# Kernel tuning notes

Measured on AMD Instinct MI355X. Metric: run time of the kernel, lower is better.

Reference implementation:

```python
import jax, jax.numpy as jnp
import numpy as np

N = 6144      # num_sample / nodes per graph
E = 196608    # edges per graph (avg degree 32)
F = 256       # input feature dim (same for all 4 graphs)
H = 256       # hidden_channels (== F so all SAGEConv layers are HxH)
D = 512       # fusion dim (hardcoded in module)
G = 4         # number of graphs
ATT = 128     # attention bottleneck (hardcoded)
WS = 0.05     # weight init scale


def setup_inputs() -> dict:
    key = jax.random.key(0)
    k = jax.random.split(key, 16)
    return {
        "xs": jax.random.normal(k[0], (G, N, F), jnp.float32),
        "edge_index": jax.random.randint(k[1], (G, 2, E), 0, N),
        "x_content": jax.random.normal(k[2], (N, F), jnp.float32),
        # SAGEConv params: per graph, 3 layers, lin_l (with bias) on aggregated
        # neighbors, lin_r (no bias) on root. F == H so all layers stack.
        "sage_Wl": jax.random.normal(k[3], (G, 3, H, H), jnp.float32) * WS,
        "sage_bl": jnp.zeros((G, 3, H), jnp.float32),
        "sage_Wr": jax.random.normal(k[4], (G, 3, H, H), jnp.float32) * WS,
        # lin1..lin4 : F -> 512
        "lin_W": jax.random.normal(k[5], (G, D, F), jnp.float32) * WS,
        "lin_b": jnp.zeros((G, D), jnp.float32),
        # ResidualFusion attention MLP 512 -> 128 -> 1, softmax over graph axis
        "att_W1": jax.random.normal(k[6], (ATT, D), jnp.float32) * WS,
        "att_b1": jnp.zeros((ATT,), jnp.float32),
        "att_W2": jax.random.normal(k[7], (1, ATT), jnp.float32) * WS,
        "att_b2": jnp.zeros((1,), jnp.float32),
        "res_W": jax.random.normal(k[8], (D, D), jnp.float32) * WS,
        "res_b": jnp.zeros((D,), jnp.float32),
        "fusion_weight": jnp.array([0.7, 0.3], jnp.float32),
        # SelfExpression coefficients, init 1e-8 * ones as in the module
        "C_content": jnp.full((N, N), 1e-8, jnp.float32),
        "C_structure": jnp.full((N, N), 1e-8, jnp.float32),
    }


def _gnn(x, ei, Wl, bl, Wr):
    # One GraphSAGE stack: 3 SAGEConv(mean) layers, relu after each,
    # dropout is identity in eval mode.
    src, dst = ei[0], ei[1]
    deg = jax.ops.segment_sum(jnp.ones((E,), x.dtype), dst, num_segments=N)
    deg = jnp.maximum(deg, 1.0)[:, None]
    for i in range(3):
        m = jax.ops.segment_sum(x[src], dst, num_segments=N) / deg  # mean aggr
        x = jax.nn.relu(m @ Wl[i].T + bl[i] + x @ Wr[i].T)
    return x


def reference(xs, edge_index, x_content, sage_Wl, sage_bl, sage_Wr,
              lin_W, lin_b, att_W1, att_b1, att_W2, att_b2,
              res_W, res_b, fusion_weight, C_content, C_structure):
    # Four GraphSAGE stacks, vmapped over the graph axis.
    xg = jax.vmap(_gnn)(xs, edge_index, sage_Wl, sage_bl, sage_Wr)  # [G,N,F]
    # lin1..lin4 -> [G,N,D]
    feats = jnp.einsum('gnf,gdf->gnd', xg, lin_W) + lin_b[:, None, :]
    # ResidualFusion: attention over stacked features, softmax over graph axis
    h = jax.nn.relu(jnp.einsum('gnd,kd->gnk', feats, att_W1) + att_b1)
    logits = jnp.einsum('gnk,ok->gno', h, att_W2) + att_b2  # [G,N,1]
    w = jax.nn.softmax(logits, axis=0)
    weighted = jnp.sum(w * feats, axis=0)            # [N,D]
    residual = feats[0] @ res_W.T + res_b            # [N,D]
    structure_features = jax.nn.relu(weighted + residual)
    # Coefficient fusion with softmax-normalized scalar weights
    fw = jax.nn.softmax(fusion_weight)
    fusion_expression = fw[0] * C_content + fw[1] * C_structure  # [N,N]
    return (fusion_expression, x_content, structure_features, C_content, C_structure)
```

## Files before the change

kernel.cpp:

```cpp
#include <hip/hip_runtime.h>
#include <hip/hip_bf16.h>

constexpr int N_ = 6144;
constexpr int E_ = 196608;
constexpr int F_ = 256;
constexpr int D_ = 512;
constexpr int G_ = 4;
constexpr int A_ = 128;

typedef short bf16x8 __attribute__((ext_vector_type(8)));
typedef float f32x4 __attribute__((ext_vector_type(4)));
typedef float f4 __attribute__((ext_vector_type(4)));
typedef int i4 __attribute__((ext_vector_type(4)));
typedef __hip_bfloat16 hb;

__device__ inline float b2f(unsigned short u) {
    union { unsigned u32; float f; } x; x.u32 = ((unsigned)u) << 16; return x.f;
}
__device__ inline unsigned short f2bu(float f) {
    hb b = __float2bfloat16(f);
    return *reinterpret_cast<unsigned short*>(&b);
}

#define GLD_LDS16(gp, lp) \
    __builtin_amdgcn_global_load_lds((const __attribute__((address_space(1))) void*)(gp), \
                                     (__attribute__((address_space(3))) void*)(lp), 16, 0, 0)

struct SP {
    const f4* Cc; const f4* Cs; const float* fw;
    f4* o0; f4* o3; f4* o4;
    long ib; long ie; int nsb;
};

__device__ void stream_slice(const SP sp, int sb)
{
    float fa = sp.fw[0], fb = sp.fw[1];
    float mx = fmaxf(fa, fb);
    float ea = expf(fa - mx), eb = expf(fb - mx);
    float w0 = ea / (ea + eb), w1 = eb / (ea + eb);
    const long S = (long)sp.nsb * blockDim.x;
    long i = sp.ib + (long)sb * blockDim.x + threadIdx.x;
    for (; i + 3 * S < sp.ie; i += 4 * S) {
        f4 a0 = __builtin_nontemporal_load(sp.Cc + i);
        f4 b0 = __builtin_nontemporal_load(sp.Cs + i);
        f4 a1 = __builtin_nontemporal_load(sp.Cc + i + S);
        f4 b1 = __builtin_nontemporal_load(sp.Cs + i + S);
        f4 a2 = __builtin_nontemporal_load(sp.Cc + i + 2 * S);
        f4 b2 = __builtin_nontemporal_load(sp.Cs + i + 2 * S);
        f4 a3 = __builtin_nontemporal_load(sp.Cc + i + 3 * S);
        f4 b3 = __builtin_nontemporal_load(sp.Cs + i + 3 * S);
        __builtin_nontemporal_store(a0, sp.o3 + i);
        __builtin_nontemporal_store(b0, sp.o4 + i);
        __builtin_nontemporal_store(w0 * a0 + w1 * b0, sp.o0 + i);
        __builtin_nontemporal_store(a1, sp.o3 + i + S);
        __builtin_nontemporal_store(b1, sp.o4 + i + S);
        __builtin_nontemporal_store(w0 * a1 + w1 * b1, sp.o0 + i + S);
        __builtin_nontemporal_store(a2, sp.o3 + i + 2 * S);
        __builtin_nontemporal_store(b2, sp.o4 + i + 2 * S);
        __builtin_nontemporal_store(w0 * a2 + w1 * b2, sp.o0 + i + 2 * S);
        __builtin_nontemporal_store(a3, sp.o3 + i + 3 * S);
        __builtin_nontemporal_store(b3, sp.o4 + i + 3 * S);
        __builtin_nontemporal_store(w0 * a3 + w1 * b3, sp.o0 + i + 3 * S);
    }
    for (; i < sp.ie; i += S) {
        f4 a = __builtin_nontemporal_load(sp.Cc + i);
        f4 b = __builtin_nontemporal_load(sp.Cs + i);
        __builtin_nontemporal_store(a, sp.o3 + i);
        __builtin_nontemporal_store(b, sp.o4 + i);
        __builtin_nontemporal_store(w0 * a + w1 * b, sp.o0 + i);
    }
}

__global__ void k_tail(SP sp) { stream_slice(sp, blockIdx.x); }

__global__ void k_prep(const float* __restrict__ xc, f4* __restrict__ o1,
                       const float* __restrict__ xs, ushort4* __restrict__ xsb,
                       const float* __restrict__ Wl, ushort4* __restrict__ Wlb,
                       const float* __restrict__ Wr, ushort4* __restrict__ Wrb,
                       const float* __restrict__ lin, ushort4* __restrict__ linb,
                       const float* __restrict__ aw, ushort4* __restrict__ awb,
                       const float* __restrict__ rw, ushort4* __restrict__ rwb,
                       i4* __restrict__ cursz, int PB, SP sp)
{
    if ((int)blockIdx.x >= PB) { stream_slice(sp, blockIdx.x - PB); return; }
    const long nz = (long)G_ * N_ / 4;
    const long n0 = (long)N_ * F_ / 4;
    const long n1 = (long)G_ * N_ * F_ / 4;
    const long n2 = (long)G_ * 3 * F_ * F_ / 4;
    const long n4 = (long)G_ * D_ * F_ / 4;
    const long n5 = (long)A_ * D_ / 4;
    const long n6 = (long)D_ * D_ / 4;
    const long T = nz + n0 + n1 + 2 * n2 + n4 + n5 + n6;
    long stride = (long)PB * blockDim.x;
    for (long u = (long)blockIdx.x * blockDim.x + threadIdx.x; u < T; u += stride) {
        long v = u;
        if (v < nz) { cursz[v] = i4{0, 0, 0, 0}; continue; }
        v -= nz;
        if (v < n0) {
            f4 x = __builtin_nontemporal_load((const f4*)xc + v);
            __builtin_nontemporal_store(x, o1 + v);
            continue;
        }
        v -= n0;
        const float* s; ushort4* d;
        if (v < n1) { s = xs; d = xsb; }
        else {
            v -= n1;
            if (v < n2) { s = Wl; d = Wlb; }
            else {
                v -= n2;
                if (v < n2) { s = Wr; d = Wrb; }
                else {
                    v -= n2;
                    if (v < n4) { s = lin; d = linb; }
                    else {
                        v -= n4;
                        if (v < n5) { s = aw; d = awb; }
                        else { v -= n5; s = rw; d = rwb; }
                    }
                }
            }
        }
        f4 x = *((const f4*)s + v);
        ushort4 o;
        o.x = f2bu(x[0]); o.y = f2bu(x[1]); o.z = f2bu(x[2]); o.w = f2bu(x[3]);
        d[v] = o;
    }
}

__global__ void k_count(const int* __restrict__ ei, int* __restrict__ cnt, SP sp)
{
    if ((int)blockIdx.x >= G_ * E_ / 256) { stream_slice(sp, blockIdx.x - G_ * E_ / 256); return; }
    long i = (long)blockIdx.x * blockDim.x + threadIdx.x;
    int g = (int)(i / E_);
    int e = (int)(i % E_);
    int dst = ei[(long)g * 2 * E_ + E_ + e];
    atomicAdd(&cnt[g * N_ + dst], 1);
}

__global__ void k_scan(int* __restrict__ cnt_cursor, int* __restrict__ row_ptr,
                       float* __restrict__ deg, SP sp)
{
    if ((int)blockIdx.x >= G_) { stream_slice(sp, blockIdx.x - G_); return; }
    int g = blockIdx.x;
    __shared__ int sdata[1024];
    __shared__ int s_off;
    if (threadIdx.x == 0) s_off = 0;
    __syncthreads();
    for (int base = 0; base < N_; base += 1024) {
        int idx = g * N_ + base + threadIdx.x;
        int v = cnt_cursor[idx];
        sdata[threadIdx.x] = v;
        __syncthreads();
        for (int d = 1; d < 1024; d <<= 1) {
            int t = (threadIdx.x >= d) ? sdata[threadIdx.x - d] : 0;
            __syncthreads();
            sdata[threadIdx.x] += t;
            __syncthreads();
        }
        int incl = sdata[threadIdx.x];
        int excl = incl - v;
        int rp = s_off + excl;
        row_ptr[g * (N_ + 1) + base + threadIdx.x] = rp;
        cnt_cursor[idx] = rp;
        deg[idx] = (float)(v > 1 ? v : 1);
        __syncthreads();
        if (threadIdx.x == 1023) s_off += incl;
        __syncthreads();
    }
    if (threadIdx.x == 0) row_ptr[g * (N_ + 1) + N_] = s_off;
}

__global__ void k_fill(const int* __restrict__ ei, int* __restrict__ cursor,
                       int* __restrict__ csr_src, SP sp)
{
    if ((int)blockIdx.x >= G_ * E_ / 256) { stream_slice(sp, blockIdx.x - G_ * E_ / 256); return; }
    long i = (long)blockIdx.x * blockDim.x + threadIdx.x;
    int g = (int)(i / E_);
    int e = (int)(i % E_);
    int src = ei[(long)g * 2 * E_ + e];
    int dst = ei[(long)g * 2 * E_ + E_ + e];
    int pos = atomicAdd(&cursor[g * N_ + dst], 1);
    csr_src[(long)g * E_ + pos] = src;
}

__global__ __launch_bounds__(256) void k_aggregate(
    const hb* __restrict__ x, const int* __restrict__ csr_src,
    const int* __restrict__ row_ptr, const float* __restrict__ deg,
    hb* __restrict__ m, SP sp)
{
    int b = blockIdx.x;
    if (b >= G_ * N_ / 4) { stream_slice(sp, b - G_ * N_ / 4); return; }
    int g = (b & 7) >> 1;
    int idx = ((b >> 3) << 1) | (b & 1);
    int node = idx * 4 + (threadIdx.x >> 6);
    int lane = threadIdx.x & 63;
    int qq = lane >> 4;
    int l16 = (lane & 15) * 16;
    const hb* xg = x + (long)g * N_ * F_;
    const int* rp = row_ptr + g * (N_ + 1);
    const int* cs = csr_src + (long)g * E_;
    int s = __builtin_amdgcn_readfirstlane(rp[node]);
    int e = __builtin_amdgcn_readfirstlane(rp[node + 1]);
    float a[16] = {};
    #pragma unroll 2
    for (int j = s; j < e; j += 4) {
        if (j + qq < e) {
            int src = cs[j + qq];
            const bf16x8* p = (const bf16x8*)(xg + (long)src * F_ + l16);
            bf16x8 v0 = p[0], v1 = p[1];
            #pragma unroll
            for (int q = 0; q < 8; ++q) a[q]     += b2f((unsigned short)v0[q]);
            #pragma unroll
            for (int q = 0; q < 8; ++q) a[q + 8] += b2f((unsigned short)v1[q]);
        }
    }
    #pragma unroll
    for (int q = 0; q < 16; ++q) {
        a[q] += __shfl_xor(a[q], 16);
        a[q] += __shfl_xor(a[q], 32);
    }
    if (qq == 0) {
        float inv = 1.0f / deg[g * N_ + node];
        bf16x8 lo, hi;
        #pragma unroll
        for (int q = 0; q < 8; ++q) { lo[q] = (short)f2bu(a[q] * inv); hi[q] = (short)f2bu(a[q + 8] * inv); }
        *(bf16x8*)(m + ((long)g * N_ + node) * F_ + l16) = lo;
        *(bf16x8*)(m + ((long)g * N_ + node) * F_ + l16 + 8) = hi;
    }
}

template <bool DUAL, bool RELU, bool LOGITS, bool FUSEOUT, bool PIN>
__global__ __launch_bounds__(256) void k_mfma_nt(
    const hb* __restrict__ A1, const hb* __restrict__ B1,
    const hb* __restrict__ A2, const hb* __restrict__ B2,
    const float* __restrict__ bias, hb* __restrict__ C,
    int ncols, int nrows, int ng, int Nc, int K,
    long a_batch, long b_batch, long bias_batch, long c_batch,
    const float* __restrict__ W2, const float* __restrict__ b2,
    float* __restrict__ logits,
    const float* __restrict__ lgAll, const hb* __restrict__ fAll,
    float* __restrict__ o2,
    SP sp)
{
    const int nComp = ncols * nrows * ng;
    int b = blockIdx.x;
    if (b >= nComp) { stream_slice(sp, b - nComp); return; }
    int g, col, row;
    if (PIN) {
        g = (b & 7) >> 1;
        int idx = ((b >> 3) << 1) | (b & 1);
        col = idx % ncols; row = idx / ncols;
    } else {
        col = b % ncols;
        int r2 = b / ncols;
        row = r2 % nrows; g = r2 / nrows;
    }
    const int row0 = row * 128;
    const int col0 = col * 128;

    const hb* A1p = A1 + (long)g * a_batch;
    const hb* B1p = B1 + (long)g * b_batch;
    const hb* A2p = nullptr;
    const hb* B2p = nullptr;
    if (DUAL) { A2p = A2 + (long)g * a_batch; B2p = B2 + (long)g * b_batch; }
    const float* biasp = bias + (long)g * bias_batch;
    hb* Cp = C + (long)g * c_batch;

    __shared__ hb As[128 * 64];
    __shared__ hb Bs[128 * 64];
    __shared__ float sLog[2][128];
    __shared__ float sW[128][4];

    const int tid = threadIdx.x;
    const int lane = tid & 63;
    const int wid = tid >> 6;
    const int wr = wid >> 1;
    const int wc = wid & 1;

    if (FUSEOUT) {
        if (tid < 128) {
            int rr = row0 + tid;
            float l0 = lgAll[rr], l1 = lgAll[N_ + rr], l2 = lgAll[2 * N_ + rr], l3 = lgAll[3 * N_ + rr];
            float mx = fmaxf(fmaxf(l0, l1), fmaxf(l2, l3));
            float e0 = expf(l0 - mx), e1 = expf(l1 - mx), e2 = expf(l2 - mx), e3 = expf(l3 - mx);
            float inv = 1.f / (e0 + e1 + e2 + e3);
            sW[tid][0] = e0 * inv; sW[tid][1] = e1 * inv;
            sW[tid][2] = e2 * inv; sW[tid][3] = e3 * inv;
        }
    }

    const int srow = tid >> 3;
    const int sk8  = (tid & 7) * 8;

    f32x4 acc[4][4] = {};

    const int fr  = lane & 15;
    const int fkq = (lane >> 4) * 8;

    const int npass = DUAL ? 2 : 1;
    for (int pass = 0; pass < npass; ++pass) {
        const hb* A = (DUAL && pass) ? A2p : A1p;
        const hb* B = (DUAL && pass) ? B2p : B1p;
        for (int k0 = 0; k0 < K; k0 += 64) {
            __syncthreads();
            #pragma unroll
            for (int c = 0; c < 4; ++c) {
                int r = c * 32 + srow;
                GLD_LDS16(A + (long)(row0 + r) * K + k0 + sk8, As + r * 64 + sk8);
                GLD_LDS16(B + (long)(col0 + r) * K + k0 + sk8, Bs + r * 64 + sk8);
            }
            __syncthreads();

            bf16x8 af[4][2], bfr[4][2];
            #pragma unroll
            for (int m = 0; m < 4; ++m)
                #pragma unroll
                for (int kk = 0; kk < 2; ++kk)
                    af[m][kk] = *(const bf16x8*)(As + (wr * 64 + m * 16 + fr) * 64 + kk * 32 + fkq);
            #pragma unroll
            for (int n = 0; n < 4; ++n)
                #pragma unroll
                for (int kk = 0; kk < 2; ++kk)
                    bfr[n][kk] = *(const bf16x8*)(Bs + (wc * 64 + n * 16 + fr) * 64 + kk * 32 + fkq);

            #pragma unroll
            for (int m = 0; m < 4; ++m)
                #pragma unroll
                for (int n = 0; n < 4; ++n)
                    #pragma unroll
                    for (int kk = 0; kk < 2; ++kk)
                        acc[m][n] = __builtin_amdgcn_mfma_f32_16x16x32_bf16(
                            af[m][kk], bfr[n][kk], acc[m][n], 0, 0, 0);
        }
    }

    const int r4 = (lane >> 4) * 4;
    const int cc = lane & 15;

    if (LOGITS) {
        float w2v[4], bv[4];
        #pragma unroll
        for (int n = 0; n < 4; ++n) {
            int c2 = wc * 64 + n * 16 + cc;
            w2v[n] = W2[c2];
            bv[n]  = biasp[c2];
        }
        #pragma unroll
        for (int m = 0; m < 4; ++m) {
            #pragma unroll
            for (int j = 0; j < 4; ++j) {
                float p = 0.f;
                #pragma unroll
                for (int n = 0; n < 4; ++n) {
                    float h = fmaxf(acc[m][n][j] + bv[n], 0.f);
                    p += h * w2v[n];
                }
                p += __shfl_xor(p, 1); p += __shfl_xor(p, 2);
                p += __shfl_xor(p, 4); p += __shfl_xor(p, 8);
                if (cc == 0) sLog[wc][wr * 64 + m * 16 + r4 + j] = p;
            }
        }
        __syncthreads();
        if (tid < 128)
            logits[(long)g * N_ + row0 + tid] = sLog[0][tid] + sLog[1][tid] + b2[0];
    } else if (FUSEOUT) {
        const unsigned short* fu = (const unsigned short*)fAll;
        #pragma unroll
        for (int m = 0; m < 4; ++m) {
            #pragma unroll
            for (int n = 0; n < 4; ++n) {
                int c2 = col0 + wc * 64 + n * 16 + cc;
                float bv = biasp[c2];
                #pragma unroll
                for (int j = 0; j < 4; ++j) {
                    int rl = wr * 64 + m * 16 + r4 + j;
                    int rr = row0 + rl;
                    float s = acc[m][n][j] + bv;
                    #pragma unroll
                    for (int gg = 0; gg < 4; ++gg)
                        s += sW[rl][gg] * b2f(fu[((long)gg * N_ + rr) * D_ + c2]);
                    __builtin_nontemporal_store(fmaxf(s, 0.f), o2 + (long)rr * D_ + c2);
                }
            }
        }
    } else {
        #pragma unroll
        for (int m = 0; m < 4; ++m) {
            #pragma unroll
            for (int n = 0; n < 4; ++n) {
                int c2 = col0 + wc * 64 + n * 16 + cc;
                float bv = biasp[c2];
                #pragma unroll
                for (int j = 0; j < 4; ++j) {
                    int rr = row0 + wr * 64 + m * 16 + r4 + j;
                    float v = acc[m][n][j] + bv;
                    if (RELU) v = fmaxf(v, 0.f);
                    Cp[(long)rr * Nc + c2] = __float2bfloat16(v);
                }
            }
        }
    }
}

extern "C" void kernel_launch(void* const* d_in, const int* in_sizes, int n_in,
                              void* d_out, int out_size, void* d_ws, size_t ws_size,
                              hipStream_t stream)
{
    const float* xs        = (const float*)d_in[0];
    const int*   ei        = (const int*)  d_in[1];
    const float* x_content = (const float*)d_in[2];
    const float* sage_Wl   = (const float*)d_in[3];
    const float* sage_bl   = (const float*)d_in[4];
    const float* sage_Wr   = (const float*)d_in[5];
    const float* lin_W     = (const float*)d_in[6];
    const float* lin_b     = (const float*)d_in[7];
    const float* att_W1    = (const float*)d_in[8];
    const float* att_b1    = (const float*)d_in[9];
    const float* att_W2    = (const float*)d_in[10];
    const float* att_b2    = (const float*)d_in[11];
    const float* res_W     = (const float*)d_in[12];
    const float* res_b     = (const float*)d_in[13];
    const float* fusion_w  = (const float*)d_in[14];
    const float* Cc        = (const float*)d_in[15];
    const float* Cs        = (const float*)d_in[16];

    float* out0 = (float*)d_out;
    float* out1 = out0 + (size_t)N_ * N_;
    float* out2 = out1 + (size_t)N_ * F_;
    float* out3 = out2 + (size_t)N_ * D_;
    float* out4 = out3 + (size_t)N_ * N_;

    char* w = (char*)d_ws;
    auto alloc = [&](size_t bytes) {
        char* p = w;
        w += (bytes + 255) & ~(size_t)255;
        return p;
    };
    hb* xsb   = (hb*)alloc((size_t)G_ * N_ * F_ * 2);
    hb* xA    = (hb*)alloc((size_t)G_ * N_ * F_ * 2);
    hb* xB    = (hb*)alloc((size_t)G_ * N_ * F_ * 2);
    hb* mb    = (hb*)alloc((size_t)G_ * N_ * F_ * 2);
    hb* feats = (hb*)alloc((size_t)G_ * N_ * D_ * 2);
    hb* Wlb   = (hb*)alloc((size_t)G_ * 3 * F_ * F_ * 2);
    hb* Wrb   = (hb*)alloc((size_t)G_ * 3 * F_ * F_ * 2);
    hb* linWb = (hb*)alloc((size_t)G_ * D_ * F_ * 2);
    hb* attWb = (hb*)alloc((size_t)A_ * D_ * 2);
    hb* resWb = (hb*)alloc((size_t)D_ * D_ * 2);
    float* logit = (float*)alloc((size_t)G_ * N_ * 4);
    float* deg   = (float*)alloc((size_t)G_ * N_ * 4);
    int*   rowp  = (int*)  alloc((size_t)G_ * (N_ + 1) * 4);
    int*   curs  = (int*)  alloc((size_t)G_ * N_ * 4);
    int*   csrc  = (int*)  alloc((size_t)G_ * E_ * 4);

    const long U = (long)N_ * N_ / 4;
    const int cum[14] = {0, 100, 115, 123, 143, 183, 233, 273, 323, 363, 413, 468, 648, 898};
    long B[14];
    for (int i = 0; i < 14; ++i) B[i] = U * cum[i] / 1000;
    const int PREPB   = 512;
    const int SB_PREP = 512;
    const int SB_FLAT = 256;
    const int SB_GEMM = 256;
    const int SB_ATT  = 768;
    const int SB_RES  = 1024;
    const int TAILB   = 1024;
    auto mkSP = [&](int i, int nsb) {
        SP sp;
        sp.Cc = (const f4*)Cc; sp.Cs = (const f4*)Cs; sp.fw = fusion_w;
        sp.o0 = (f4*)out0; sp.o3 = (f4*)out3; sp.o4 = (f4*)out4;
        sp.ib = B[i]; sp.ie = (i == 13) ? U : B[i + 1]; sp.nsb = nsb;
        return sp;
    };
    SP tail = mkSP(13, TAILB);

    k_prep<<<PREPB + SB_PREP, 256, 0, stream>>>(
        x_content, (f4*)out1, xs, (ushort4*)xsb,
        sage_Wl, (ushort4*)Wlb, sage_Wr, (ushort4*)Wrb,
        lin_W, (ushort4*)linWb, att_W1, (ushort4*)attWb, res_W, (ushort4*)resWb,
        (i4*)curs, PREPB, mkSP(0, SB_PREP));

    k_count<<<G_ * E_ / 256 + SB_FLAT, 256, 0, stream>>>(ei, curs, mkSP(1, SB_FLAT));
    k_scan<<<G_ + SB_FLAT, 1024, 0, stream>>>(curs, rowp, deg, mkSP(2, SB_FLAT));
    k_fill<<<G_ * E_ / 256 + SB_FLAT, 256, 0, stream>>>(ei, curs, csrc, mkSP(3, SB_FLAT));

    const hb* xin = xsb;
    hb* xout = xA;
    for (int layer = 0; layer < 3; ++layer) {
        k_aggregate<<<G_ * N_ / 4 + SB_FLAT, 256, 0, stream>>>(
            xin, csrc, rowp, deg, mb, mkSP(4 + 2 * layer, SB_FLAT));
        k_mfma_nt<true, true, false, false, true>
            <<<(F_ / 128) * (N_ / 128) * G_ + SB_GEMM, 256, 0, stream>>>(
            mb, Wlb + (size_t)layer * F_ * F_,
            xin, Wrb + (size_t)layer * F_ * F_,
            sage_bl + (size_t)layer * F_, xout,
            F_ / 128, N_ / 128, G_, F_, F_,
            (long)N_ * F_, (long)3 * F_ * F_, (long)3 * F_, (long)N_ * F_,
            nullptr, nullptr, nullptr, nullptr, nullptr, nullptr,
            mkSP(5 + 2 * layer, SB_GEMM));
        xin = xout;
        xout = (layer == 0) ? xB : xA;
    }
    const hb* xg = xA;

    k_mfma_nt<false, false, false, false, true>
        <<<(D_ / 128) * (N_ / 128) * G_ + SB_GEMM, 256, 0, stream>>>(
        xg, linWb, nullptr, nullptr, lin_b, feats,
        D_ / 128, N_ / 128, G_, D_, F_,
        (long)N_ * F_, (long)D_ * F_, (long)D_, (long)N_ * D_,
        nullptr, nullptr, nullptr, nullptr, nullptr, nullptr,
        mkSP(10, SB_GEMM));

    k_mfma_nt<false, true, true, false, true>
        <<<(A_ / 128) * (N_ / 128) * G_ + SB_ATT, 256, 0, stream>>>(
        feats, attWb, nullptr, nullptr, att_b1, nullptr,
        A_ / 128, N_ / 128, G_, A_, D_,
        (long)N_ * D_, 0L, 0L, 0L,
        att_W2, att_b2, logit, nullptr, nullptr, nullptr,
        mkSP(11, SB_ATT));

    k_mfma_nt<false, false, false, true, false>
        <<<(D_ / 128) * (N_ / 128) * 1 + SB_RES, 256, 0, stream>>>(
        feats, resWb, nullptr, nullptr, res_b, nullptr,
        D_ / 128, N_ / 128, 1, D_, D_,
        0L, 0L, 0L, 0L,
        nullptr, nullptr, nullptr, logit, feats, out2,
        mkSP(12, SB_RES));

    k_tail<<<TAILB, 256, 0, stream>>>(tail);
}
```

Before: 433.9 us.

## Replace static copy-stream slices with atomic work-stealing chunks across all kernels

The large N×N coefficient copy/blend stream was split into hand-tuned fixed fractions per kernel launch. It is now claimed in 16K-float4 chunks through a global atomic cursor that every kernel's extra blocks, and compute blocks once their own work is done, drain dynamically. The aim is to balance the bandwidth-bound stream against compute phases without hand-tuned ratios and to shrink the final tail kernel. This costs an atomic and two block barriers per chunk, and compute blocks may linger in the stream and delay the next dependent launch.

```diff
diff --git a/kernel.cpp b/kernel.cpp
--- a/kernel.cpp
+++ b/kernel.cpp
@@ -8,6 +8,10 @@
 constexpr int G_ = 4;
 constexpr int A_ = 128;
 
+constexpr int CHUNK_F4 = 16384;
+constexpr long U_F4 = (long)N_ * N_ / 4;
+constexpr int NCHUNK = (int)(U_F4 / CHUNK_F4);
+
 typedef short bf16x8 __attribute__((ext_vector_type(8)));
 typedef float f32x4 __attribute__((ext_vector_type(4)));
 typedef float f4 __attribute__((ext_vector_type(4)));
@@ -26,52 +30,54 @@
     __builtin_amdgcn_global_load_lds((const __attribute__((address_space(1))) void*)(gp), \
                                      (__attribute__((address_space(3))) void*)(lp), 16, 0, 0)
 
-struct SP {
+struct SW {
     const f4* Cc; const f4* Cs; const float* fw;
     f4* o0; f4* o3; f4* o4;
-    long ib; long ie; int nsb;
+    int* cursor;
 };
 
-__device__ void stream_slice(const SP sp, int sb)
-{
-    float fa = sp.fw[0], fb = sp.fw[1];
+__device__ void stream_steal(const SW sw)
+{
+    __shared__ int s_c;
+    float fa = sw.fw[0], fb = sw.fw[1];
     float mx = fmaxf(fa, fb);
     float ea = expf(fa - mx), eb = expf(fb - mx);
     float w0 = ea / (ea + eb), w1 = eb / (ea + eb);
-    const long S = (long)sp.nsb * blockDim.x;
-    long i = sp.ib + (long)sb * blockDim.x + threadIdx.x;
-    for (; i + 3 * S < sp.ie; i += 4 * S) {
-        f4 a0 = __builtin_nontemporal_load(sp.Cc + i);
-        f4 b0 = __builtin_nontemporal_load(sp.Cs + i);
-        f4 a1 = __builtin_nontemporal_load(sp.Cc + i + S);
-        f4 b1 = __builtin_nontemporal_load(sp.Cs + i + S);
-        f4 a2 = __builtin_nontemporal_load(sp.Cc + i + 2 * S);
-        f4 b2 = __builtin_nontemporal_load(sp.Cs + i + 2 * S);
-        f4 a3 = __builtin_nontemporal_load(sp.Cc + i + 3 * S);
-        f4 b3 = __builtin_nontemporal_load(sp.Cs + i + 3 * S);
-        __builtin_nontemporal_store(a0, sp.o3 + i);
-        __builtin_nontemporal_store(b0, sp.o4 + i);
-        __builtin_nontemporal_store(w0 * a0 + w1 * b0, sp.o0 + i);
-        __builtin_nontemporal_store(a1, sp.o3 + i + S);
-        __builtin_nontemporal_store(b1, sp.o4 + i + S);
-        __builtin_nontemporal_store(w0 * a1 + w1 * b1, sp.o0 + i + S);
-        __builtin_nontemporal_store(a2, sp.o3 + i + 2 * S);
-        __builtin_nontemporal_store(b2, sp.o4 + i + 2 * S);
-        __builtin_nontemporal_store(w0 * a2 + w1 * b2, sp.o0 + i + 2 * S);
-        __builtin_nontemporal_store(a3, sp.o3 + i + 3 * S);
-        __builtin_nontemporal_store(b3, sp.o4 + i + 3 * S);
-        __builtin_nontemporal_store(w0 * a3 + w1 * b3, sp.o0 + i + 3 * S);
-    }
-    for (; i < sp.ie; i += S) {
-        f4 a = __builtin_nontemporal_load(sp.Cc + i);
-        f4 b = __builtin_nontemporal_load(sp.Cs + i);
-        __builtin_nontemporal_store(a, sp.o3 + i);
-        __builtin_nontemporal_store(b, sp.o4 + i);
-        __builtin_nontemporal_store(w0 * a + w1 * b, sp.o0 + i);
-    }
-}
-
-__global__ void k_tail(SP sp) { stream_slice(sp, blockIdx.x); }
+    const long S = blockDim.x;
+    while (true) {
+        __syncthreads();
+        if (threadIdx.x == 0) s_c = atomicAdd(sw.cursor, 1);
+        __syncthreads();
+        int c = s_c;
+        if (c >= NCHUNK) return;
+        const long base = (long)c * CHUNK_F4;
+        const long end  = base + CHUNK_F4;
+        for (long i = base + threadIdx.x; i < end; i += 4 * S) {
+            f4 a0 = __builtin_nontemporal_load(sw.Cc + i);
+            f4 b0 = __builtin_nontemporal_load(sw.Cs + i);
+            f4 a1 = __builtin_nontemporal_load(sw.Cc + i + S);
+            f4 b1 = __builtin_nontemporal_load(sw.Cs + i + S);
+            f4 a2 = __builtin_nontemporal_load(sw.Cc + i + 2 * S);
+            f4 b2 = __builtin_nontemporal_load(sw.Cs + i + 2 * S);
+            f4 a3 = __builtin_nontemporal_load(sw.Cc + i + 3 * S);
+            f4 b3 = __builtin_nontemporal_load(sw.Cs + i + 3 * S);
+            __builtin_nontemporal_store(a0, sw.o3 + i);
+            __builtin_nontemporal_store(b0, sw.o4 + i);
+            __builtin_nontemporal_store(w0 * a0 + w1 * b0, sw.o0 + i);
+            __builtin_nontemporal_store(a1, sw.o3 + i + S);
+            __builtin_nontemporal_store(b1, sw.o4 + i + S);
+            __builtin_nontemporal_store(w0 * a1 + w1 * b1, sw.o0 + i + S);
+            __builtin_nontemporal_store(a2, sw.o3 + i + 2 * S);
+            __builtin_nontemporal_store(b2, sw.o4 + i + 2 * S);
+            __builtin_nontemporal_store(w0 * a2 + w1 * b2, sw.o0 + i + 2 * S);
+            __builtin_nontemporal_store(a3, sw.o3 + i + 3 * S);
+            __builtin_nontemporal_store(b3, sw.o4 + i + 3 * S);
+            __builtin_nontemporal_store(w0 * a3 + w1 * b3, sw.o0 + i + 3 * S);
+        }
+    }
+}
+
+__global__ void k_drain(SW sw) { stream_steal(sw); }
 
 __global__ void k_prep(const float* __restrict__ xc, f4* __restrict__ o1,
                        const float* __restrict__ xs, ushort4* __restrict__ xsb,
@@ -80,9 +86,9 @@
                        const float* __restrict__ lin, ushort4* __restrict__ linb,
                        const float* __restrict__ aw, ushort4* __restrict__ awb,
                        const float* __restrict__ rw, ushort4* __restrict__ rwb,
-                       i4* __restrict__ cursz, int PB, SP sp)
-{
-    if ((int)blockIdx.x >= PB) { stream_slice(sp, blockIdx.x - PB); return; }
+                       i4* __restrict__ cursz, int PB, SW sw)
+{
+    if ((int)blockIdx.x >= PB) { stream_steal(sw); return; }
     const long nz = (long)G_ * N_ / 4;
     const long n0 = (long)N_ * F_ / 4;
     const long n1 = (long)G_ * N_ * F_ / 4;
@@ -126,22 +132,25 @@
         o.x = f2bu(x[0]); o.y = f2bu(x[1]); o.z = f2bu(x[2]); o.w = f2bu(x[3]);
         d[v] = o;
     }
-}
-
-__global__ void k_count(const int* __restrict__ ei, int* __restrict__ cnt, SP sp)
-{
-    if ((int)blockIdx.x >= G_ * E_ / 256) { stream_slice(sp, blockIdx.x - G_ * E_ / 256); return; }
-    long i = (long)blockIdx.x * blockDim.x + threadIdx.x;
-    int g = (int)(i / E_);
-    int e = (int)(i % E_);
-    int dst = ei[(long)g * 2 * E_ + E_ + e];
-    atomicAdd(&cnt[g * N_ + dst], 1);
+    stream_steal(sw);
+}
+
+__global__ void k_count(const int* __restrict__ ei, int* __restrict__ cnt, SW sw)
+{
+    if ((int)blockIdx.x < G_ * E_ / 256) {
+        long i = (long)blockIdx.x * blockDim.x + threadIdx.x;
+        int g = (int)(i / E_);
+        int e = (int)(i % E_);
+        int dst = ei[(long)g * 2 * E_ + E_ + e];
+        atomicAdd(&cnt[g * N_ + dst], 1);
+    }
+    stream_steal(sw);
 }
 
 __global__ void k_scan(int* __restrict__ cnt_cursor, int* __restrict__ row_ptr,
-                       float* __restrict__ deg, SP sp)
-{
-    if ((int)blockIdx.x >= G_) { stream_slice(sp, blockIdx.x - G_); return; }
+                       float* __restrict__ deg, SW sw)
+{
+    if ((int)blockIdx.x >= G_) { stream_steal(sw); return; }
     int g = blockIdx.x;
     __shared__ int sdata[1024];
     __shared__ int s_off;
@@ -169,65 +178,71 @@
         __syncthreads();
     }
     if (threadIdx.x == 0) row_ptr[g * (N_ + 1) + N_] = s_off;
+    stream_steal(sw);
 }
 
 __global__ void k_fill(const int* __restrict__ ei, int* __restrict__ cursor,
-                       int* __restrict__ csr_src, SP sp)
-{
-    if ((int)blockIdx.x >= G_ * E_ / 256) { stream_slice(sp, blockIdx.x - G_ * E_ / 256); return; }
-    long i = (long)blockIdx.x * blockDim.x + threadIdx.x;
-    int g = (int)(i / E_);
-    int e = (int)(i % E_);
-    int src = ei[(long)g * 2 * E_ + e];
-    int dst = ei[(long)g * 2 * E_ + E_ + e];
-    int pos = atomicAdd(&cursor[g * N_ + dst], 1);
-    csr_src[(long)g * E_ + pos] = src;
+                       int* __restrict__ csr_src, SW sw)
+{
+    if ((int)blockIdx.x < G_ * E_ / 256) {
+        long i = (long)blockIdx.x * blockDim.x + threadIdx.x;
+        int g = (int)(i / E_);
+        int e = (int)(i % E_);
+        int src = ei[(long)g * 2 * E_ + e];
+        int dst = ei[(long)g * 2 * E_ + E_ + e];
+        int pos = atomicAdd(&cursor[g * N_ + dst], 1);
+        csr_src[(long)g * E_ + pos] = src;
+    }
+    stream_steal(sw);
 }
 
 __global__ __launch_bounds__(256) void k_aggregate(
     const hb* __restrict__ x, const int* __restrict__ csr_src,
     const int* __restrict__ row_ptr, const float* __restrict__ deg,
-    hb* __restrict__ m, SP sp)
+    hb* __restrict__ m, SW sw)
 {
     int b = blockIdx.x;
-    if (b >= G_ * N_ / 4) { stream_slice(sp, b - G_ * N_ / 4); return; }
-    int g = (b & 7) >> 1;
-    int idx = ((b >> 3) << 1) | (b & 1);
-    int node = idx * 4 + (threadIdx.x >> 6);
-    int lane = threadIdx.x & 63;
-    int qq = lane >> 4;
-    int l16 = (lane & 15) * 16;
-    const hb* xg = x + (long)g * N_ * F_;
-    const int* rp = row_ptr + g * (N_ + 1);
-    const int* cs = csr_src + (long)g * E_;
-    int s = __builtin_amdgcn_readfirstlane(rp[node]);
-    int e = __builtin_amdgcn_readfirstlane(rp[node + 1]);
-    float a[16] = {};
-    #pragma unroll 2
-    for (int j = s; j < e; j += 4) {
-        if (j + qq < e) {
-            int src = cs[j + qq];
-            const bf16x8* p = (const bf16x8*)(xg + (long)src * F_ + l16);
-            bf16x8 v0 = p[0], v1 = p[1];
-            #pragma unroll
-            for (int q = 0; q < 8; ++q) a[q]     += b2f((unsigned short)v0[q]);
-            #pragma unroll
-            for (int q = 0; q < 8; ++q) a[q + 8] += b2f((unsigned short)v1[q]);
-        }
-    }
-    #pragma unroll
-    for (int q = 0; q < 16; ++q) {
-        a[q] += __shfl_xor(a[q], 16);
-        a[q] += __shfl_xor(a[q], 32);
-    }
-    if (qq == 0) {
-        float inv = 1.0f / deg[g * N_ + node];
-        bf16x8 lo, hi;
+    if (b >= G_ * N_ / 4) { stream_steal(sw); return; }
+    {
+        int g = (b & 7) >> 1;
+        int idx = ((b >> 3) << 1) | (b & 1);
+        int node = idx * 4 + (threadIdx.x >> 6);
+        int lane = threadIdx.x & 63;
+        int qq = lane >> 4;
+        int l16 = (lane & 15) * 16;
+        const hb* xg = x + (long)g * N_ * F_;
+        const int* rp = row_ptr + g * (N_ + 1);
+        const int* cs = csr_src + (long)g * E_;
+        int s = __builtin_amdgcn_readfirstlane(rp[node]);
+        int e = __builtin_amdgcn_readfirstlane(rp[node + 1]);
+        float a[16] = {};
+        #pragma unroll 2
+        for (int j = s; j < e; j += 4) {
+            if (j + qq < e) {
+                int src = cs[j + qq];
+                const bf16x8* p = (const bf16x8*)(xg + (long)src * F_ + l16);
+                bf16x8 v0 = p[0], v1 = p[1];
+                #pragma unroll
+                for (int q = 0; q < 8; ++q) a[q]     += b2f((unsigned short)v0[q]);
+                #pragma unroll
+                for (int q = 0; q < 8; ++q) a[q + 8] += b2f((unsigned short)v1[q]);
+            }
+        }
         #pragma unroll
-        for (int q = 0; q < 8; ++q) { lo[q] = (short)f2bu(a[q] * inv); hi[q] = (short)f2bu(a[q + 8] * inv); }
-        *(bf16x8*)(m + ((long)g * N_ + node) * F_ + l16) = lo;
-        *(bf16x8*)(m + ((long)g * N_ + node) * F_ + l16 + 8) = hi;
-    }
+        for (int q = 0; q < 16; ++q) {
+            a[q] += __shfl_xor(a[q], 16);
+            a[q] += __shfl_xor(a[q], 32);
+        }
+        if (qq == 0) {
+            float inv = 1.0f / deg[g * N_ + node];
+            bf16x8 lo, hi;
+            #pragma unroll
+            for (int q = 0; q < 8; ++q) { lo[q] = (short)f2bu(a[q] * inv); hi[q] = (short)f2bu(a[q + 8] * inv); }
+            *(bf16x8*)(m + ((long)g * N_ + node) * F_ + l16) = lo;
+            *(bf16x8*)(m + ((long)g * N_ + node) * F_ + l16 + 8) = hi;
+        }
+    }
+    stream_steal(sw);
 }
 
 template <bool DUAL, bool RELU, bool LOGITS, bool FUSEOUT, bool PIN>
@@ -241,11 +256,12 @@
     float* __restrict__ logits,
     const float* __restrict__ lgAll, const hb* __restrict__ fAll,
     float* __restrict__ o2,
-    SP sp)
+    SW sw)
 {
     const int nComp = ncols * nrows * ng;
     int b = blockIdx.x;
-    if (b >= nComp) { stream_slice(sp, b - nComp); return; }
+    if (b >= nComp) { stream_steal(sw); return; }
+    {
     int g, col, row;
     if (PIN) {
         g = (b & 7) >> 1;
@@ -401,6 +417,8 @@
             }
         }
     }
+    }
+    stream_steal(sw);
 }
 
 extern "C" void kernel_launch(void* const* d_in, const int* in_sizes, int n_in,
@@ -452,79 +470,66 @@
     int*   rowp  = (int*)  alloc((size_t)G_ * (N_ + 1) * 4);
     int*   curs  = (int*)  alloc((size_t)G_ * N_ * 4);
     int*   csrc  = (int*)  alloc((size_t)G_ * E_ * 4);
-
-    const long U = (long)N_ * N_ / 4;
-    const int cum[14] = {0, 100, 115, 123, 143, 183, 233, 273, 323, 363, 413, 468, 648, 898};
-    long B[14];
-    for (int i = 0; i < 14; ++i) B[i] = U * cum[i] / 1000;
-    const int PREPB   = 512;
-    const int SB_PREP = 512;
-    const int SB_FLAT = 256;
-    const int SB_GEMM = 256;
-    const int SB_ATT  = 768;
-    const int SB_RES  = 1024;
-    const int TAILB   = 1024;
-    auto mkSP = [&](int i, int nsb) {
-        SP sp;
-        sp.Cc = (const f4*)Cc; sp.Cs = (const f4*)Cs; sp.fw = fusion_w;
-        sp.o0 = (f4*)out0; sp.o3 = (f4*)out3; sp.o4 = (f4*)out4;
-        sp.ib = B[i]; sp.ie = (i == 13) ? U : B[i + 1]; sp.nsb = nsb;
-        return sp;
-    };
-    SP tail = mkSP(13, TAILB);
-
-    k_prep<<<PREPB + SB_PREP, 256, 0, stream>>>(
+    int*   scur  = (int*)  alloc(256);
+
+    SW sw;
+    sw.Cc = (const f4*)Cc; sw.Cs = (const f4*)Cs; sw.fw = fusion_w;
+    sw.o0 = (f4*)out0; sw.o3 = (f4*)out3; sw.o4 = (f4*)out4;
+    sw.cursor = scur;
+
+    const int PREPB = 512;
+    const int SB    = 768;
+
+    hipMemsetAsync(scur, 0, 4, stream);
+
+    k_prep<<<PREPB + SB, 256, 0, stream>>>(
         x_content, (f4*)out1, xs, (ushort4*)xsb,
         sage_Wl, (ushort4*)Wlb, sage_Wr, (ushort4*)Wrb,
         lin_W, (ushort4*)linWb, att_W1, (ushort4*)attWb, res_W, (ushort4*)resWb,
-        (i4*)curs, PREPB, mkSP(0, SB_PREP));
-
-    k_count<<<G_ * E_ / 256 + SB_FLAT, 256, 0, stream>>>(ei, curs, mkSP(1, SB_FLAT));
-    k_scan<<<G_ + SB_FLAT, 1024, 0, stream>>>(curs, rowp, deg, mkSP(2, SB_FLAT));
-    k_fill<<<G_ * E_ / 256 + SB_FLAT, 256, 0, stream>>>(ei, curs, csrc, mkSP(3, SB_FLAT));
+        (i4*)curs, PREPB, sw);
+
+    k_count<<<G_ * E_ / 256 + SB, 256, 0, stream>>>(ei, curs, sw);
+    k_scan<<<G_ + 256, 1024, 0, stream>>>(curs, rowp, deg, sw);
+    k_fill<<<G_ * E_ / 256 + SB, 256, 0, stream>>>(ei, curs, csrc, sw);
 
     const hb* xin = xsb;
     hb* xout = xA;
     for (int layer = 0; layer < 3; ++layer) {
-        k_aggregate<<<G_ * N_ / 4 + SB_FLAT, 256, 0, stream>>>(
-            xin, csrc, rowp, deg, mb, mkSP(4 + 2 * layer, SB_FLAT));
+        k_aggregate<<<G_ * N_ / 4 + SB, 256, 0, stream>>>(
+            xin, csrc, rowp, deg, mb, sw);
         k_mfma_nt<true, true, false, false, true>
-            <<<(F_ / 128) * (N_ / 128) * G_ + SB_GEMM, 256, 0, stream>>>(
+            <<<(F_ / 128) * (N_ / 128) * G_ + SB, 256, 0, stream>>>(
             mb, Wlb + (size_t)layer * F_ * F_,
             xin, Wrb + (size_t)layer * F_ * F_,
             sage_bl + (size_t)layer * F_, xout,
             F_ / 128, N_ / 128, G_, F_, F_,
             (long)N_ * F_, (long)3 * F_ * F_, (long)3 * F_, (long)N_ * F_,
-            nullptr, nullptr, nullptr, nullptr, nullptr, nullptr,
-            mkSP(5 + 2 * layer, SB_GEMM));
+            nullptr, nullptr, nullptr, nullptr, nullptr, nullptr, sw);
         xin = xout;
         xout = (layer == 0) ? xB : xA;
     }
     const hb* xg = xA;
 
     k_mfma_nt<false, false, false, false, true>
-        <<<(D_ / 128) * (N_ / 128) * G_ + SB_GEMM, 256, 0, stream>>>(
+        <<<(D_ / 128) * (N_ / 128) * G_ + SB, 256, 0, stream>>>(
         xg, linWb, nullptr, nullptr, lin_b, feats,
         D_ / 128, N_ / 128, G_, D_, F_,
         (long)N_ * F_, (long)D_ * F_, (long)D_, (long)N_ * D_,
-        nullptr, nullptr, nullptr, nullptr, nullptr, nullptr,
-        mkSP(10, SB_GEMM));
+        nullptr, nullptr, nullptr, nullptr, nullptr, nullptr, sw);
 
     k_mfma_nt<false, true, true, false, true>
-        <<<(A_ / 128) * (N_ / 128) * G_ + SB_ATT, 256, 0, stream>>>(
+        <<<(A_ / 128) * (N_ / 128) * G_ + SB, 256, 0, stream>>>(
         feats, attWb, nullptr, nullptr, att_b1, nullptr,
         A_ / 128, N_ / 128, G_, A_, D_,
         (long)N_ * D_, 0L, 0L, 0L,
-        att_W2, att_b2, logit, nullptr, nullptr, nullptr,
-        mkSP(11, SB_ATT));
+        att_W2, att_b2, logit, nullptr, nullptr, nullptr, sw);
 
     k_mfma_nt<false, false, false, true, false>
-        <<<(D_ / 128) * (N_ / 128) * 1 + SB_RES, 256, 0, stream>>>(
+        <<<(D_ / 128) * (N_ / 128) * 1 + SB, 256, 0, stream>>>(
         feats, resWb, nullptr, nullptr, res_b, nullptr,
         D_ / 128, N_ / 128, 1, D_, D_,
         0L, 0L, 0L, 0L,
-        nullptr, nullptr, nullptr, logit, feats, out2,
-        mkSP(12, SB_RES));
-
-    k_tail<<<TAILB, 256, 0, stream>>>(tail);
-}
+        nullptr, nullptr, nullptr, logit, feats, out2, sw);
+
+    k_drain<<<2048, 256, 0, stream>>>(sw);
+}
```

After: 753.5 us. +73.6%, slower.
